# Performance work log

Measured on AMD Instinct MI355X. Metric: run time of the kernel, lower is better.

## Reference

```python
import jax, jax.numpy as jnp
import numpy as np

E = 524288
B = 16
NODE_IN = 128
EDGE_IN = 64
GLOBAL_IN = 64
HIDDEN = 256
EDGE_OUT = 64
CAT_IN = EDGE_IN + 2 * NODE_IN + GLOBAL_IN  # 384


def setup_inputs() -> dict:
    key = jax.random.key(0)
    ks = jax.random.split(key, 9)
    src = jax.random.normal(ks[0], (E, NODE_IN), dtype=jnp.float32)
    dest = jax.random.normal(ks[1], (E, NODE_IN), dtype=jnp.float32)
    edge_attr = jax.random.normal(ks[2], (E, EDGE_IN), dtype=jnp.float32)
    u = jax.random.normal(ks[3], (B, GLOBAL_IN), dtype=jnp.float32)
    batch = jnp.sort(jax.random.randint(ks[4], (E,), 0, B, dtype=jnp.int64))
    # MLP params (torch Linear default init scale ~1/sqrt(fan_in))
    W1 = jax.random.normal(ks[5], (CAT_IN, HIDDEN), dtype=jnp.float32) / np.sqrt(CAT_IN)
    b1 = jax.random.normal(ks[6], (HIDDEN,), dtype=jnp.float32) / np.sqrt(CAT_IN)
    W2 = jax.random.normal(ks[7], (HIDDEN, EDGE_OUT), dtype=jnp.float32) / np.sqrt(HIDDEN)
    b2 = jax.random.normal(ks[8], (EDGE_OUT,), dtype=jnp.float32) / np.sqrt(HIDDEN)
    return {"src": src, "dest": dest, "edge_attr": edge_attr, "u": u,
            "batch": batch, "W1": W1, "b1": b1, "W2": W2, "b2": b2}


def reference(src, dest, edge_attr, u, batch, W1, b1, W2, b2):
    # gather global features per edge, concat, 2-layer MLP with ReLU
    x = jnp.concatenate([src, dest, edge_attr, u[batch]], axis=1)  # [E, 384]
    h = jax.nn.relu(x @ W1 + b1)                                   # [E, hidden]
    return h @ W2 + b2                                             # [E, edge_out]
```

## Files before the change

### kernel.cpp

```cpp
#include <hip/hip_runtime.h>

typedef __bf16 bf16_t;
typedef bf16_t bf16x8 __attribute__((ext_vector_type(8)));
typedef bf16_t bf16x4 __attribute__((ext_vector_type(4)));
typedef float f32x4 __attribute__((ext_vector_type(4)));
typedef unsigned short u16;
typedef unsigned int u32;

#define E_TOT 524288
#define MT 64
#define NBLK (E_TOT / MT)

__device__ __forceinline__ u16 f2bf(float f) {
  u32 u = __builtin_bit_cast(u32, f);
  u += 0x7FFFu + ((u >> 16) & 1u);
  return (u16)(u >> 16);
}

__device__ __forceinline__ bf16x8 pack8(f32x4 a, f32x4 b) {
  bf16x8 p;
  p[0] = (bf16_t)a[0]; p[1] = (bf16_t)a[1]; p[2] = (bf16_t)a[2]; p[3] = (bf16_t)a[3];
  p[4] = (bf16_t)b[0]; p[5] = (bf16_t)b[1]; p[6] = (bf16_t)b[2]; p[7] = (bf16_t)b[3];
  return p;
}

__global__ void prep_w1f(const float* __restrict__ W1, u16* __restrict__ W1F) {
  int t = blockIdx.x * 256 + threadIdx.x;
  if (t < 98304) {
    int e  = t & 7;
    int l  = (t >> 3) & 63;
    int nf = (t >> 9) & 3;
    int wc = (t >> 11) & 3;
    int kb = t >> 13;
    int n = wc * 64 + nf * 16 + (l & 15);
    int k = kb * 32 + ((l >> 4) << 3) + e;
    W1F[t] = f2bf(W1[k * 256 + n]);
  }
}

__global__ void prep_w2f(const float* __restrict__ W2, u16* __restrict__ W2F) {
  int t = blockIdx.x * 256 + threadIdx.x;
  if (t < 16384) {
    int e   = t & 7;
    int l   = (t >> 3) & 63;
    int n2f = (t >> 9) & 3;
    int ks  = t >> 11;
    int n2 = n2f * 16 + (l & 15);
    int k  = ks * 32 + ((l >> 4) << 3) + e;
    W2F[t] = f2bf(W2[k * 64 + n2]);
  }
}

__global__ void __launch_bounds__(256) edge_fused(
    const float* __restrict__ src, const float* __restrict__ dst,
    const float* __restrict__ ea, const float* __restrict__ u,
    const int* __restrict__ batch, const u16* __restrict__ W1F,
    const float* __restrict__ b1, const u16* __restrict__ W2F,
    const float* __restrict__ b2, float* __restrict__ out)
{
  __shared__ __align__(16) u16 smem[16384];
  u16* As = smem;
  u16* Hs = smem;

  const int t    = threadIdx.x;
  const int wid  = t >> 6;
  const int lane = t & 63;
  const int lr   = lane & 15;
  const int lg   = lane >> 4;
  const int e0   = blockIdx.x * MT;
  const int r    = t >> 2;
  const int jcol = t & 3;
  const int bidx = batch[e0 + r];
  const int wunit = r * 4 + (jcol ^ ((r >> 1) & 3));

  auto loadA = [&](int c, f32x4* ra) {
    const float* p;
    if (c < 4)       p = src + (size_t)(e0 + r) * 128 + c * 32 + jcol * 8;
    else if (c < 8)  p = dst + (size_t)(e0 + r) * 128 + (c - 4) * 32 + jcol * 8;
    else if (c < 10) p = ea + (size_t)(e0 + r) * 64 + (c - 8) * 32 + jcol * 8;
    else             p = u + (size_t)bidx * 64 + (c - 10) * 32 + jcol * 8;
    ra[0] = *(const f32x4*)p;
    ra[1] = *(const f32x4*)(p + 4);
  };
  auto loadW1 = [&](int c, bf16x8* wf) {
    const u16* p = W1F + ((size_t)(c * 4 + wid) * 4) * 512 + lane * 8;
    wf[0] = *(const bf16x8*)(p);
    wf[1] = *(const bf16x8*)(p + 512);
    wf[2] = *(const bf16x8*)(p + 1024);
    wf[3] = *(const bf16x8*)(p + 1536);
  };

  f32x4 ra[2], rb[2];
  bf16x8 wA[4], wB[4];
  loadA(0, ra);
  loadW1(0, wA);
  loadA(1, rb);
  loadW1(1, wB);

  f32x4 acc[4][4];
  #pragma unroll
  for (int i = 0; i < 4; ++i)
    #pragma unroll
    for (int j = 0; j < 4; ++j)
      acc[i][j] = (f32x4){0.f, 0.f, 0.f, 0.f};

  #pragma unroll
  for (int kb = 0; kb < 12; ++kb) {
    f32x4*  rc = (kb & 1) ? rb : ra;
    bf16x8* wc_ = (kb & 1) ? wB : wA;
    u16* Ab = As + (kb & 1) * 2048;

    *(bf16x8*)&Ab[wunit * 8] = pack8(rc[0], rc[1]);
    if (kb <= 9) loadA(kb + 2, rc);
    __syncthreads();

    __builtin_amdgcn_s_setprio(1);
    bf16x8 af[4];
    #pragma unroll
    for (int mf = 0; mf < 4; ++mf) {
      int row = mf * 16 + lr;
      af[mf] = *(const bf16x8*)&Ab[(row * 4 + (lg ^ ((row >> 1) & 3))) * 8];
    }
    #pragma unroll
    for (int nf = 0; nf < 4; ++nf)
      #pragma unroll
      for (int mf = 0; mf < 4; ++mf)
        acc[nf][mf] = __builtin_amdgcn_mfma_f32_16x16x32_bf16(wc_[nf], af[mf], acc[nf][mf], 0, 0, 0);
    __builtin_amdgcn_s_setprio(0);

    if (kb <= 9) loadW1(kb + 2, wc_);
  }
  __syncthreads();

  #pragma unroll
  for (int nf = 0; nf < 4; ++nf) {
    f32x4 b1v = *(const f32x4*)(b1 + wid * 64 + nf * 16 + lg * 4);
    #pragma unroll
    for (int mf = 0; mf < 4; ++mf) {
      int row = mf * 16 + lr;
      bf16x4 hb;
      #pragma unroll
      for (int rr = 0; rr < 4; ++rr)
        hb[rr] = (bf16_t)fmaxf(acc[nf][mf][rr] + b1v[rr], 0.f);
      int uu = (wid * 4 + nf) * 4 + lg;
      int up = uu ^ ((row & 3) << 3);
      *(bf16x4*)&Hs[row * 256 + up * 4] = hb;
    }
  }
  __syncthreads();

  const int row2 = wid * 16 + lr;
  f32x4 d2[4];
  #pragma unroll
  for (int i = 0; i < 4; ++i) d2[i] = (f32x4){0.f, 0.f, 0.f, 0.f};
  #pragma unroll
  for (int ks = 0; ks < 8; ++ks) {
    int uu = ks * 8 + lg * 2;
    int up = uu ^ ((row2 & 3) << 3);
    bf16x8 a2 = *(const bf16x8*)&Hs[row2 * 256 + up * 4];
    const u16* q = W2F + (size_t)ks * 2048 + lane * 8;
    #pragma unroll
    for (int n2f = 0; n2f < 4; ++n2f)
      d2[n2f] = __builtin_amdgcn_mfma_f32_16x16x32_bf16(
          *(const bf16x8*)(q + n2f * 512), a2, d2[n2f], 0, 0, 0);
  }

  #pragma unroll
  for (int n2f = 0; n2f < 4; ++n2f) {
    f32x4 b2v = *(const f32x4*)(b2 + n2f * 16 + lg * 4);
    f32x4 ov = d2[n2f] + b2v;
    *(f32x4*)&out[(size_t)(e0 + row2) * 64 + n2f * 16 + lg * 4] = ov;
  }
}

extern "C" void kernel_launch(void* const* d_in, const int* in_sizes, int n_in,
                              void* d_out, int out_size, void* d_ws, size_t ws_size,
                              hipStream_t stream) {
  const float* src  = (const float*)d_in[0];
  const float* dst  = (const float*)d_in[1];
  const float* ea   = (const float*)d_in[2];
  const float* u    = (const float*)d_in[3];
  const int* batch  = (const int*)d_in[4];
  const float* W1   = (const float*)d_in[5];
  const float* b1   = (const float*)d_in[6];
  const float* W2   = (const float*)d_in[7];
  const float* b2   = (const float*)d_in[8];
  float* out = (float*)d_out;

  u16* W1F = (u16*)d_ws;
  u16* W2F = W1F + 98304;

  prep_w1f<<<384, 256, 0, stream>>>(W1, W1F);
  prep_w2f<<<64, 256, 0, stream>>>(W2, W2F);
  edge_fused<<<NBLK, 256, 0, stream>>>(src, dst, ea, u, batch, W1F, b1, W2F, b2, out);
}
```

Baseline: 234.7 us.

## Widen K-step to 64 with single-buffered prefetch and new LDS swizzles

The GEMM1 K loop now processes 64 columns per iteration (6 iterations instead of 12), loading 16 floats per thread per step. The two register double-buffers for A and W1 fragments become a single prefetch buffer. The intent is to halve the number of barriers and raise MFMA work per synchronisation. The __syncthreads is replaced by an explicit lgkmcnt wait, s_barrier and sched_barrier, and the A-tile and H-tile XOR swizzles are changed to cut LDS bank conflicts. In exchange the prefetch distance drops from two steps to one, which exposes more global-load latency, and the wider loads raise register pressure.

```diff
diff --git a/kernel.cpp b/kernel.cpp
--- a/kernel.cpp
+++ b/kernel.cpp
@@ -69,33 +69,36 @@
   const int lg   = lane >> 4;
   const int e0   = blockIdx.x * MT;
   const int r    = t >> 2;
-  const int jcol = t & 3;
+  const int jc   = t & 3;
   const int bidx = batch[e0 + r];
-  const int wunit = r * 4 + (jcol ^ ((r >> 1) & 3));
+  const int u0   = 2 * jc;
 
   auto loadA = [&](int c, f32x4* ra) {
     const float* p;
-    if (c < 4)       p = src + (size_t)(e0 + r) * 128 + c * 32 + jcol * 8;
-    else if (c < 8)  p = dst + (size_t)(e0 + r) * 128 + (c - 4) * 32 + jcol * 8;
-    else if (c < 10) p = ea + (size_t)(e0 + r) * 64 + (c - 8) * 32 + jcol * 8;
-    else             p = u + (size_t)bidx * 64 + (c - 10) * 32 + jcol * 8;
+    if (c < 2)       p = src + (size_t)(e0 + r) * 128 + c * 64 + jc * 16;
+    else if (c < 4)  p = dst + (size_t)(e0 + r) * 128 + (c - 2) * 64 + jc * 16;
+    else if (c == 4) p = ea + (size_t)(e0 + r) * 64 + jc * 16;
+    else             p = u + (size_t)bidx * 64 + jc * 16;
     ra[0] = *(const f32x4*)p;
     ra[1] = *(const f32x4*)(p + 4);
+    ra[2] = *(const f32x4*)(p + 8);
+    ra[3] = *(const f32x4*)(p + 12);
   };
   auto loadW1 = [&](int c, bf16x8* wf) {
-    const u16* p = W1F + ((size_t)(c * 4 + wid) * 4) * 512 + lane * 8;
-    wf[0] = *(const bf16x8*)(p);
-    wf[1] = *(const bf16x8*)(p + 512);
-    wf[2] = *(const bf16x8*)(p + 1024);
-    wf[3] = *(const bf16x8*)(p + 1536);
+    #pragma unroll
+    for (int ks = 0; ks < 2; ++ks) {
+      const u16* p = W1F + ((size_t)((2 * c + ks) * 4 + wid) * 4) * 512 + lane * 8;
+      wf[ks * 4 + 0] = *(const bf16x8*)(p);
+      wf[ks * 4 + 1] = *(const bf16x8*)(p + 512);
+      wf[ks * 4 + 2] = *(const bf16x8*)(p + 1024);
+      wf[ks * 4 + 3] = *(const bf16x8*)(p + 1536);
+    }
   };
 
-  f32x4 ra[2], rb[2];
-  bf16x8 wA[4], wB[4];
+  f32x4 ra[4];
+  bf16x8 wf[8];
   loadA(0, ra);
-  loadW1(0, wA);
-  loadA(1, rb);
-  loadW1(1, wB);
+  loadW1(0, wf);
 
   f32x4 acc[4][4];
   #pragma unroll
@@ -105,30 +108,39 @@
       acc[i][j] = (f32x4){0.f, 0.f, 0.f, 0.f};
 
   #pragma unroll
-  for (int kb = 0; kb < 12; ++kb) {
-    f32x4*  rc = (kb & 1) ? rb : ra;
-    bf16x8* wc_ = (kb & 1) ? wB : wA;
-    u16* Ab = As + (kb & 1) * 2048;
-
-    *(bf16x8*)&Ab[wunit * 8] = pack8(rc[0], rc[1]);
-    if (kb <= 9) loadA(kb + 2, rc);
-    __syncthreads();
+  for (int kb = 0; kb < 6; ++kb) {
+    u16* Ab = As + (kb & 1) * 4096;
+
+    {
+      bf16x8 lo = pack8(ra[0], ra[1]);
+      bf16x8 hi = pack8(ra[2], ra[3]);
+      *(bf16x8*)&Ab[(r * 8 + (u0 ^ (r & 7))) * 8]       = lo;
+      *(bf16x8*)&Ab[(r * 8 + ((u0 + 1) ^ (r & 7))) * 8] = hi;
+    }
+    if (kb < 5) loadA(kb + 1, ra);
+
+    asm volatile("s_waitcnt lgkmcnt(0)" ::: "memory");
+    __builtin_amdgcn_s_barrier();
+    __builtin_amdgcn_sched_barrier(0);
 
     __builtin_amdgcn_s_setprio(1);
-    bf16x8 af[4];
-    #pragma unroll
-    for (int mf = 0; mf < 4; ++mf) {
-      int row = mf * 16 + lr;
-      af[mf] = *(const bf16x8*)&Ab[(row * 4 + (lg ^ ((row >> 1) & 3))) * 8];
-    }
-    #pragma unroll
-    for (int nf = 0; nf < 4; ++nf)
+    #pragma unroll
+    for (int ks = 0; ks < 2; ++ks) {
+      bf16x8 af[4];
       #pragma unroll
-      for (int mf = 0; mf < 4; ++mf)
-        acc[nf][mf] = __builtin_amdgcn_mfma_f32_16x16x32_bf16(wc_[nf], af[mf], acc[nf][mf], 0, 0, 0);
+      for (int mf = 0; mf < 4; ++mf) {
+        int row = mf * 16 + lr;
+        af[mf] = *(const bf16x8*)&Ab[(row * 8 + ((ks * 4 + lg) ^ (row & 7))) * 8];
+      }
+      #pragma unroll
+      for (int nf = 0; nf < 4; ++nf)
+        #pragma unroll
+        for (int mf = 0; mf < 4; ++mf)
+          acc[nf][mf] = __builtin_amdgcn_mfma_f32_16x16x32_bf16(wf[ks * 4 + nf], af[mf], acc[nf][mf], 0, 0, 0);
+    }
     __builtin_amdgcn_s_setprio(0);
 
-    if (kb <= 9) loadW1(kb + 2, wc_);
+    if (kb < 5) loadW1(kb + 1, wf);
   }
   __syncthreads();
 
@@ -143,7 +155,7 @@
       for (int rr = 0; rr < 4; ++rr)
         hb[rr] = (bf16_t)fmaxf(acc[nf][mf][rr] + b1v[rr], 0.f);
       int uu = (wid * 4 + nf) * 4 + lg;
-      int up = uu ^ ((row & 3) << 3);
+      int up = uu ^ ((lr & 3) << 2);
       *(bf16x4*)&Hs[row * 256 + up * 4] = hb;
     }
   }
@@ -156,7 +168,7 @@
   #pragma unroll
   for (int ks = 0; ks < 8; ++ks) {
     int uu = ks * 8 + lg * 2;
-    int up = uu ^ ((row2 & 3) << 3);
+    int up = uu ^ ((lr & 3) << 2);
     bf16x8 a2 = *(const bf16x8*)&Hs[row2 * 256 + up * 4];
     const u16* q = W2F + (size_t)ks * 2048 + lane * 8;
     #pragma unroll
```

After: 243.6 us. 1.04x slower.

## Load A fragments directly from global into registers, drop LDS staging and barriers

Applied to the files above, without the earlier changes.

Removes the LDS round-trip for the concatenated input tile. Each wave now loads its own MFMA A fragments straight from global memory and converts them to bf16 in registers, which eliminates the per-k-block __syncthreads and LDS writes and reads. In exchange every wave redundantly loads the full 64-row A tile, four times the global or L2 traffic, and loses the explicit double-buffered prefetch of inputs and W1. The H-buffer swizzle is also changed to a different XOR pattern.

```diff
diff --git a/kernel.cpp b/kernel.cpp
--- a/kernel.cpp
+++ b/kernel.cpp
@@ -58,9 +58,7 @@
     const float* __restrict__ b1, const u16* __restrict__ W2F,
     const float* __restrict__ b2, float* __restrict__ out)
 {
-  __shared__ __align__(16) u16 smem[16384];
-  u16* As = smem;
-  u16* Hs = smem;
+  __shared__ __align__(16) u16 Hs[16384];
 
   const int t    = threadIdx.x;
   const int wid  = t >> 6;
@@ -68,34 +66,14 @@
   const int lr   = lane & 15;
   const int lg   = lane >> 4;
   const int e0   = blockIdx.x * MT;
-  const int r    = t >> 2;
-  const int jcol = t & 3;
-  const int bidx = batch[e0 + r];
-  const int wunit = r * 4 + (jcol ^ ((r >> 1) & 3));
+  const int kk   = lg << 3;
 
-  auto loadA = [&](int c, f32x4* ra) {
-    const float* p;
-    if (c < 4)       p = src + (size_t)(e0 + r) * 128 + c * 32 + jcol * 8;
-    else if (c < 8)  p = dst + (size_t)(e0 + r) * 128 + (c - 4) * 32 + jcol * 8;
-    else if (c < 10) p = ea + (size_t)(e0 + r) * 64 + (c - 8) * 32 + jcol * 8;
-    else             p = u + (size_t)bidx * 64 + (c - 10) * 32 + jcol * 8;
-    ra[0] = *(const f32x4*)p;
-    ra[1] = *(const f32x4*)(p + 4);
-  };
-  auto loadW1 = [&](int c, bf16x8* wf) {
-    const u16* p = W1F + ((size_t)(c * 4 + wid) * 4) * 512 + lane * 8;
-    wf[0] = *(const bf16x8*)(p);
-    wf[1] = *(const bf16x8*)(p + 512);
-    wf[2] = *(const bf16x8*)(p + 1024);
-    wf[3] = *(const bf16x8*)(p + 1536);
-  };
-
-  f32x4 ra[2], rb[2];
-  bf16x8 wA[4], wB[4];
-  loadA(0, ra);
-  loadW1(0, wA);
-  loadA(1, rb);
-  loadW1(1, wB);
+  int er[4], bidx[4];
+  #pragma unroll
+  for (int mf = 0; mf < 4; ++mf) {
+    er[mf]   = e0 + mf * 16 + lr;
+    bidx[mf] = batch[er[mf]];
+  }
 
   f32x4 acc[4][4];
   #pragma unroll
@@ -105,45 +83,47 @@
       acc[i][j] = (f32x4){0.f, 0.f, 0.f, 0.f};
 
   #pragma unroll
-  for (int kb = 0; kb < 12; ++kb) {
-    f32x4*  rc = (kb & 1) ? rb : ra;
-    bf16x8* wc_ = (kb & 1) ? wB : wA;
-    u16* Ab = As + (kb & 1) * 2048;
+  for (int c = 0; c < 12; ++c) {
+    const u16* q = W1F + ((size_t)(c * 4 + wid) * 4) * 512 + lane * 8;
+    bf16x8 wf0 = *(const bf16x8*)(q);
+    bf16x8 wf1 = *(const bf16x8*)(q + 512);
+    bf16x8 wf2 = *(const bf16x8*)(q + 1024);
+    bf16x8 wf3 = *(const bf16x8*)(q + 1536);
 
-    *(bf16x8*)&Ab[wunit * 8] = pack8(rc[0], rc[1]);
-    if (kb <= 9) loadA(kb + 2, rc);
-    __syncthreads();
-
-    __builtin_amdgcn_s_setprio(1);
     bf16x8 af[4];
     #pragma unroll
     for (int mf = 0; mf < 4; ++mf) {
-      int row = mf * 16 + lr;
-      af[mf] = *(const bf16x8*)&Ab[(row * 4 + (lg ^ ((row >> 1) & 3))) * 8];
+      const float* p;
+      if (c < 4)       p = src + (size_t)er[mf] * 128 + c * 32 + kk;
+      else if (c < 8)  p = dst + (size_t)er[mf] * 128 + (c - 4) * 32 + kk;
+      else if (c < 10) p = ea + (size_t)er[mf] * 64 + (c - 8) * 32 + kk;
+      else             p = u + (size_t)bidx[mf] * 64 + (c - 10) * 32 + kk;
+      af[mf] = pack8(*(const f32x4*)p, *(const f32x4*)(p + 4));
     }
+
+    __builtin_amdgcn_s_setprio(1);
     #pragma unroll
-    for (int nf = 0; nf < 4; ++nf)
-      #pragma unroll
-      for (int mf = 0; mf < 4; ++mf)
-        acc[nf][mf] = __builtin_amdgcn_mfma_f32_16x16x32_bf16(wc_[nf], af[mf], acc[nf][mf], 0, 0, 0);
+    for (int mf = 0; mf < 4; ++mf) {
+      acc[0][mf] = __builtin_amdgcn_mfma_f32_16x16x32_bf16(wf0, af[mf], acc[0][mf], 0, 0, 0);
+      acc[1][mf] = __builtin_amdgcn_mfma_f32_16x16x32_bf16(wf1, af[mf], acc[1][mf], 0, 0, 0);
+      acc[2][mf] = __builtin_amdgcn_mfma_f32_16x16x32_bf16(wf2, af[mf], acc[2][mf], 0, 0, 0);
+      acc[3][mf] = __builtin_amdgcn_mfma_f32_16x16x32_bf16(wf3, af[mf], acc[3][mf], 0, 0, 0);
+    }
     __builtin_amdgcn_s_setprio(0);
-
-    if (kb <= 9) loadW1(kb + 2, wc_);
   }
-  __syncthreads();
 
   #pragma unroll
   for (int nf = 0; nf < 4; ++nf) {
     f32x4 b1v = *(const f32x4*)(b1 + wid * 64 + nf * 16 + lg * 4);
     #pragma unroll
     for (int mf = 0; mf < 4; ++mf) {
-      int row = mf * 16 + lr;
       bf16x4 hb;
       #pragma unroll
       for (int rr = 0; rr < 4; ++rr)
         hb[rr] = (bf16_t)fmaxf(acc[nf][mf][rr] + b1v[rr], 0.f);
+      int row = mf * 16 + lr;
       int uu = (wid * 4 + nf) * 4 + lg;
-      int up = uu ^ ((row & 3) << 3);
+      int up = uu ^ ((lr & 3) << 2);
       *(bf16x4*)&Hs[row * 256 + up * 4] = hb;
     }
   }
@@ -156,7 +136,7 @@
   #pragma unroll
   for (int ks = 0; ks < 8; ++ks) {
     int uu = ks * 8 + lg * 2;
-    int up = uu ^ ((row2 & 3) << 3);
+    int up = uu ^ ((lr & 3) << 2);
     bf16x8 a2 = *(const bf16x8*)&Hs[row2 * 256 + up * 4];
     const u16* q = W2F + (size_t)ks * 2048 + lane * 8;
     #pragma unroll
```

Result: slower. 419.0 us (+78.5%).

## Stream W1 tiles into LDS via async global_load_lds with deeper A prefetch

Applied to the files above, without the earlier changes.

W1 chunks are now repacked into a swizzled chunk-major layout and fetched directly into double-buffered LDS with global_load_lds, instead of each wave loading its own register fragments. The activation prefetch goes from two stages to three, with hand-set vmcnt waits and raw barriers replacing __syncthreads. The H-tile swizzle is also changed. The aim is to cut VGPR pressure and overlap W1 traffic with MFMA work. In exchange it uses more LDS, and the hand-counted vmcnt values are fragile.

```diff
diff --git a/kernel.cpp b/kernel.cpp
--- a/kernel.cpp
+++ b/kernel.cpp
@@ -24,17 +24,20 @@
   return p;
 }
 
-__global__ void prep_w1f(const float* __restrict__ W1, u16* __restrict__ W1F) {
+__device__ __forceinline__ void gload_lds16(const void* g, void* l) {
+  __builtin_amdgcn_global_load_lds(
+      (const __attribute__((address_space(1))) u32*)g,
+      (__attribute__((address_space(3))) u32*)l, 16, 0, 0);
+}
+
+__global__ void prep_w1tc(const float* __restrict__ W1, u16* __restrict__ W1Tc) {
   int t = blockIdx.x * 256 + threadIdx.x;
-  if (t < 98304) {
-    int e  = t & 7;
-    int l  = (t >> 3) & 63;
-    int nf = (t >> 9) & 3;
-    int wc = (t >> 11) & 3;
-    int kb = t >> 13;
-    int n = wc * 64 + nf * 16 + (l & 15);
-    int k = kb * 32 + ((l >> 4) << 3) + e;
-    W1F[t] = f2bf(W1[k * 256 + n]);
+  if (t < 384 * 256) {
+    int U = t >> 3, e = t & 7;
+    int c = U >> 10, rem = U & 1023;
+    int n = rem >> 2, j = rem & 3;
+    int k = c * 32 + ((j ^ ((n >> 1) & 3)) << 3) + e;
+    W1Tc[t] = f2bf(W1[k * 256 + n]);
   }
 }
 
@@ -54,12 +57,13 @@
 __global__ void __launch_bounds__(256) edge_fused(
     const float* __restrict__ src, const float* __restrict__ dst,
     const float* __restrict__ ea, const float* __restrict__ u,
-    const int* __restrict__ batch, const u16* __restrict__ W1F,
+    const int* __restrict__ batch, const u16* __restrict__ W1Tc,
     const float* __restrict__ b1, const u16* __restrict__ W2F,
     const float* __restrict__ b2, float* __restrict__ out)
 {
-  __shared__ __align__(16) u16 smem[16384];
+  __shared__ __align__(16) u16 smem[20480];
   u16* As = smem;
+  u16* Wb = smem + 4096;
   u16* Hs = smem;
 
   const int t    = threadIdx.x;
@@ -82,20 +86,20 @@
     ra[0] = *(const f32x4*)p;
     ra[1] = *(const f32x4*)(p + 4);
   };
-  auto loadW1 = [&](int c, bf16x8* wf) {
-    const u16* p = W1F + ((size_t)(c * 4 + wid) * 4) * 512 + lane * 8;
-    wf[0] = *(const bf16x8*)(p);
-    wf[1] = *(const bf16x8*)(p + 512);
-    wf[2] = *(const bf16x8*)(p + 1024);
-    wf[3] = *(const bf16x8*)(p + 1536);
+  auto issueW = [&](int c, u16* Wn) {
+    #pragma unroll
+    for (int g = 0; g < 4; ++g) {
+      int ub = wid * 256 + g * 64;
+      gload_lds16(W1Tc + ((size_t)c * 1024 + ub + lane) * 8, Wn + ub * 8);
+    }
   };
 
-  f32x4 ra[2], rb[2];
-  bf16x8 wA[4], wB[4];
-  loadA(0, ra);
-  loadW1(0, wA);
-  loadA(1, rb);
-  loadW1(1, wB);
+  f32x4 a0[2], a1[2], a2[2];
+  loadA(0, a0);
+  loadA(1, a1);
+  loadA(2, a2);
+  issueW(0, Wb);
+  issueW(1, Wb + 8192);
 
   f32x4 acc[4][4];
   #pragma unroll
@@ -106,13 +110,20 @@
 
   #pragma unroll
   for (int kb = 0; kb < 12; ++kb) {
-    f32x4*  rc = (kb & 1) ? rb : ra;
-    bf16x8* wc_ = (kb & 1) ? wB : wA;
+    f32x4* cur = (kb % 3 == 0) ? a0 : (kb % 3 == 1) ? a1 : a2;
     u16* Ab = As + (kb & 1) * 2048;
-
-    *(bf16x8*)&Ab[wunit * 8] = pack8(rc[0], rc[1]);
-    if (kb <= 9) loadA(kb + 2, rc);
-    __syncthreads();
+    u16* Wc = Wb + (kb & 1) * 8192;
+
+    *(bf16x8*)&Ab[wunit * 8] = pack8(cur[0], cur[1]);
+    if (kb <= 8) loadA(kb + 3, cur);
+
+    if (kb == 0)       asm volatile("s_waitcnt vmcnt(6) lgkmcnt(0)" ::: "memory");
+    else if (kb <= 8)  asm volatile("s_waitcnt vmcnt(8) lgkmcnt(0)" ::: "memory");
+    else if (kb == 9)  asm volatile("s_waitcnt vmcnt(6) lgkmcnt(0)" ::: "memory");
+    else if (kb == 10) asm volatile("s_waitcnt vmcnt(4) lgkmcnt(0)" ::: "memory");
+    else               asm volatile("s_waitcnt vmcnt(0) lgkmcnt(0)" ::: "memory");
+    __builtin_amdgcn_sched_barrier(0);
+    __builtin_amdgcn_s_barrier();
 
     __builtin_amdgcn_s_setprio(1);
     bf16x8 af[4];
@@ -122,15 +133,18 @@
       af[mf] = *(const bf16x8*)&Ab[(row * 4 + (lg ^ ((row >> 1) & 3))) * 8];
     }
     #pragma unroll
-    for (int nf = 0; nf < 4; ++nf)
+    for (int nf = 0; nf < 4; ++nf) {
+      int n = wid * 64 + nf * 16 + lr;
+      bf16x8 wfr = *(const bf16x8*)&Wc[(n * 4 + (lg ^ ((n >> 1) & 3))) * 8];
       #pragma unroll
       for (int mf = 0; mf < 4; ++mf)
-        acc[nf][mf] = __builtin_amdgcn_mfma_f32_16x16x32_bf16(wc_[nf], af[mf], acc[nf][mf], 0, 0, 0);
+        acc[nf][mf] = __builtin_amdgcn_mfma_f32_16x16x32_bf16(wfr, af[mf], acc[nf][mf], 0, 0, 0);
+    }
     __builtin_amdgcn_s_setprio(0);
-
-    if (kb <= 9) loadW1(kb + 2, wc_);
-  }
-  __syncthreads();
+    __builtin_amdgcn_s_barrier();
+
+    if (kb <= 9) issueW(kb + 2, Wc);
+  }
 
   #pragma unroll
   for (int nf = 0; nf < 4; ++nf) {
@@ -143,7 +157,7 @@
       for (int rr = 0; rr < 4; ++rr)
         hb[rr] = (bf16_t)fmaxf(acc[nf][mf][rr] + b1v[rr], 0.f);
       int uu = (wid * 4 + nf) * 4 + lg;
-      int up = uu ^ ((row & 3) << 3);
+      int up = uu ^ ((lr & 3) << 2);
       *(bf16x4*)&Hs[row * 256 + up * 4] = hb;
     }
   }
@@ -156,7 +170,7 @@
   #pragma unroll
   for (int ks = 0; ks < 8; ++ks) {
     int uu = ks * 8 + lg * 2;
-    int up = uu ^ ((row2 & 3) << 3);
+    int up = uu ^ ((lr & 3) << 2);
     bf16x8 a2 = *(const bf16x8*)&Hs[row2 * 256 + up * 4];
     const u16* q = W2F + (size_t)ks * 2048 + lane * 8;
     #pragma unroll
@@ -187,10 +201,10 @@
   const float* b2   = (const float*)d_in[8];
   float* out = (float*)d_out;
 
-  u16* W1F = (u16*)d_ws;
-  u16* W2F = W1F + 98304;
-
-  prep_w1f<<<384, 256, 0, stream>>>(W1, W1F);
+  u16* W1Tc = (u16*)d_ws;
+  u16* W2F  = W1Tc + 384 * 256;
+
+  prep_w1tc<<<(384 * 256 + 255) / 256, 256, 0, stream>>>(W1, W1Tc);
   prep_w2f<<<64, 256, 0, stream>>>(W2, W2F);
-  edge_fused<<<NBLK, 256, 0, stream>>>(src, dst, ea, u, batch, W1F, b1, W2F, b2, out);
-}
+  edge_fused<<<NBLK, 256, 0, stream>>>(src, dst, ea, u, batch, W1Tc, b1, W2F, b2, out);
+}
```

Measured after the change: 256.9 us. 9.4% more time.
